# Optimization experiments

Measured on AMD Instinct MI355X. Metric: run time of the kernel, lower is better.

Reference implementation:

```python
import jax, jax.numpy as jnp
import numpy as np

HIDDEN = 2048
ENGRAM = 256
ENTRIES = 32768
K = 3  # conv kernel size
LN_EPS = 1e-6
NORM_EPS = 1e-8
INV_TEMP = ENGRAM ** 0.5  # retrieval_temperature = 1/sqrt(engram_dim)
CLAMP_MIN = 0.5  # step 0 < clamp_until_step=800 -> hard clamp active


def _l2norm(x):
    n = jnp.linalg.norm(x, axis=-1, keepdims=True)
    return x / jnp.maximum(n, NORM_EPS)


def _rmsnorm(x, w, eps=LN_EPS):
    ms = jnp.mean(jnp.square(x), axis=-1, keepdims=True)
    return x * jax.lax.rsqrt(ms + eps) * w


def _layernorm(x, g, b, eps=LN_EPS):
    mu = jnp.mean(x, axis=-1, keepdims=True)
    var = jnp.mean(jnp.square(x - mu), axis=-1, keepdims=True)
    return (x - mu) * jax.lax.rsqrt(var + eps) * g + b


def setup_inputs() -> dict:
    key = jax.random.key(0)
    ks = jax.random.split(key, 7)
    s = lambda fan: 1.0 / np.sqrt(fan)
    return {
        "hidden_state": jax.random.normal(ks[0], (4, 1024, HIDDEN), jnp.float32),
        "table": jax.random.normal(ks[1], (ENTRIES, ENGRAM), jnp.float32),
        "Wq": jax.random.normal(ks[2], (HIDDEN, ENGRAM), jnp.float32) * s(HIDDEN),
        "ln_gamma": jnp.ones((ENGRAM,), jnp.float32),
        "ln_beta": jnp.zeros((ENGRAM,), jnp.float32),
        "Wk": jax.random.normal(ks[3], (ENGRAM, HIDDEN), jnp.float32) * s(ENGRAM),
        "Wv": jax.random.normal(ks[4], (ENGRAM, HIDDEN), jnp.float32) * s(ENGRAM),
        "gate_norm_w": jnp.ones((HIDDEN,), jnp.float32),
        "key_norm_w": jnp.ones((HIDDEN,), jnp.float32),
        # depthwise causal conv weight [C, K] (torch init zeros; randn for a meaningful test)
        "conv_w": jax.random.normal(ks[5], (HIDDEN, K), jnp.float32) * 0.1,
    }


def reference(hidden_state, table, Wq, ln_gamma, ln_beta, Wk, Wv,
              gate_norm_w, key_norm_w, conv_w):
    B, L, C = hidden_state.shape
    # --- retrieval: cosine-sim softmax attention over frozen table ---
    q = jnp.einsum('blc,ce->ble', hidden_state, Wq)
    qn = _l2norm(q)
    tn = _l2norm(table)
    sims = jnp.einsum('ble,te->blt', qn, tn)            # [B,L,T]
    weights = jax.nn.softmax(sims * INV_TEMP, axis=-1)
    retrieved = jnp.einsum('blt,te->ble', weights, table)
    retrieved = _layernorm(retrieved, ln_gamma, ln_beta)
    # --- key/value projections + gating ---
    key_ = jnp.einsum('ble,ec->blc', retrieved, Wk)
    value = jnp.einsum('ble,ec->blc', retrieved, Wv)
    h_norm = _rmsnorm(hidden_state, gate_norm_w)
    k_norm = _rmsnorm(key_, key_norm_w)
    dot = jnp.sum(h_norm * k_norm, axis=-1, keepdims=True)
    raw_gate = jax.nn.sigmoid(dot / np.sqrt(C).astype(np.float32))
    gate = jnp.maximum(raw_gate, CLAMP_MIN)             # clamp phase (step < 800)
    gated = gate * value                                 # [B,L,C]
    # --- causal depthwise conv along seq (left pad K-1) ---
    padded = jnp.pad(gated, ((0, 0), (K - 1, 0), (0, 0)))
    conv = sum(conv_w[:, k] * padded[:, k:k + L, :] for k in range(K))
    return jax.nn.silu(conv), gate
```

## Files before the change

kernel.cpp:

```cpp
#include <hip/hip_runtime.h>
#include <stdint.h>


#define NTOK 4096
#define CDIM 2048
#define EDIM 256
#define TROWS 32768
#define SPLIT 16
#define OUT0 (NTOK * CDIM)

typedef __attribute__((ext_vector_type(8))) short bf16x8;
typedef __attribute__((ext_vector_type(4))) float f32x4;

__device__ inline float bf2f(unsigned short u) { return __uint_as_float((unsigned)u << 16); }
__device__ inline unsigned short f2bf(float f) {
  unsigned x = __float_as_uint(f);
  x += 0x7fffu + ((x >> 16) & 1u);
  return (unsigned short)(x >> 16);
}
__device__ inline unsigned cvt_pk_bf16(float lo, float hi) {
  unsigned r;
  asm("v_cvt_pk_bf16_f32 %0, %1, %2" : "=v"(r) : "v"(lo), "v"(hi));
  return r;
}
__device__ inline void gll16(const void* g, void* l) {
  __builtin_amdgcn_global_load_lds((const __attribute__((address_space(1))) void*)g,
                                   (__attribute__((address_space(3))) void*)l, 16, 0, 0);
}

__global__ __launch_bounds__(256) void cast_bf16_kernel(
    const float* __restrict__ in, unsigned short* __restrict__ out) {
  const int idx = blockIdx.x * 256 + threadIdx.x;
  float4 v0 = *reinterpret_cast<const float4*>(&in[(size_t)idx * 8]);
  float4 v1 = *reinterpret_cast<const float4*>(&in[(size_t)idx * 8 + 4]);
  bf16x8 o;
  o[0] = (short)f2bf(v0.x); o[1] = (short)f2bf(v0.y);
  o[2] = (short)f2bf(v0.z); o[3] = (short)f2bf(v0.w);
  o[4] = (short)f2bf(v1.x); o[5] = (short)f2bf(v1.y);
  o[6] = (short)f2bf(v1.z); o[7] = (short)f2bf(v1.w);
  *reinterpret_cast<bf16x8*>(&out[(size_t)idx * 8]) = o;
}

__global__ __launch_bounds__(256) void transpose_cast_kernel(
    const float* __restrict__ in0, const float* __restrict__ in1,
    unsigned short* __restrict__ out, int R, int C) {
  __shared__ float lt[32][33];
  const int tid = threadIdx.x;
  const int r0 = blockIdx.x * 32, c0 = blockIdx.y * 32;
  const float* in = blockIdx.z ? in1 : in0;
  unsigned short* op = out + (size_t)blockIdx.z * R * C;
  {
    int r = tid >> 3, c4 = (tid & 7) * 4;
    float4 v = *reinterpret_cast<const float4*>(&in[(size_t)(r0 + r) * C + c0 + c4]);
    lt[r][c4] = v.x; lt[r][c4 + 1] = v.y; lt[r][c4 + 2] = v.z; lt[r][c4 + 3] = v.w;
  }
  __syncthreads();
  {
    int c = tid >> 3, r4 = (tid & 7) * 4;
#pragma unroll
    for (int j = 0; j < 4; ++j)
      op[(size_t)(c0 + c) * R + r0 + r4 + j] = f2bf(lt[r4 + j][c]);
  }
}

__global__ __launch_bounds__(256) void tabprep_kernel(
    const float* __restrict__ table, unsigned short* __restrict__ tnb,
    unsigned short* __restrict__ tvb) {
  __shared__ float lt[32][257];
  __shared__ float inv[32];
  const int tid = threadIdx.x, nb = blockIdx.x;
  const int r0 = nb * 32;
#pragma unroll
  for (int i = 0; i < 8; ++i) {
    int id = i * 256 + tid;
    int row = id >> 6, e4 = (id & 63) * 4;
    float4 v = *reinterpret_cast<const float4*>(&table[(size_t)(r0 + row) * EDIM + e4]);
    lt[row][e4] = v.x; lt[row][e4 + 1] = v.y; lt[row][e4 + 2] = v.z; lt[row][e4 + 3] = v.w;
  }
  __syncthreads();
  {
    int row = tid >> 3, sub = tid & 7;
    float ss = 0.f;
#pragma unroll
    for (int j = 0; j < 32; ++j) { float v = lt[row][sub + 8 * j]; ss = fmaf(v, v, ss); }
    ss += __shfl_xor(ss, 1); ss += __shfl_xor(ss, 2); ss += __shfl_xor(ss, 4);
    if (sub == 0) inv[row] = 1.f / fmaxf(sqrtf(ss), 1e-8f);
  }
  __syncthreads();
#pragma unroll
  for (int i = 0; i < 4; ++i) {
    int q = i * 256 + tid;
    {
      int c8 = q >> 5, row = q & 31;
      bf16x8 v;
#pragma unroll
      for (int j = 0; j < 8; ++j) v[j] = (short)f2bf(lt[row][c8 * 8 + j] * inv[row]);
      *reinterpret_cast<bf16x8*>(&tnb[(size_t)nb * 8192 + q * 8]) = v;
    }
    {
      int hi = q >> 8, e = q & 255;
      bf16x8 v;
#pragma unroll
      for (int j = 0; j < 8; ++j) v[j] = (short)f2bf(lt[hi * 8 + j][e]);
      *reinterpret_cast<bf16x8*>(&tvb[(size_t)nb * 8192 + q * 8]) = v;
    }
  }
}

template <bool F32OUT>
__global__ __launch_bounds__(256, 2) void gemm_bt_kernel(
    const unsigned short* __restrict__ A, const unsigned short* __restrict__ BT,
    void* __restrict__ Cout, int M, int N, int Kfull, int klen) {
  __shared__ alignas(16) unsigned short sA[2][128 * 64];
  __shared__ alignas(16) unsigned short sB[2][128 * 64];
  const int tid = threadIdx.x;
  const int lane = tid & 63;
  const int wave = tid >> 6;
  const int laneLo = lane & 15, laneHi = lane >> 4;
  const int nbn = N >> 7;
  const int bm = blockIdx.x / nbn, bn = blockIdx.x % nbn;
  const int koff = blockIdx.y * klen;
  const int wr = wave >> 1, wc = wave & 1;
  f32x4 acc[4][4];
#pragma unroll
  for (int m = 0; m < 4; ++m)
#pragma unroll
    for (int n = 0; n < 4; ++n) acc[m][n] = (f32x4){0.f, 0.f, 0.f, 0.f};
  const int nkt = klen >> 6;
  auto STAGE = [&](int b, int kt) {
#pragma unroll
    for (int i = 0; i < 4; ++i) {
      int q = i * 256 + tid;
      int row = q >> 3, cl = q & 7;
      int cs = cl ^ (row & 7);
      gll16(A + ((size_t)(bm * 128 + row) * Kfull + koff + kt * 64 + cs * 8), &sA[b][q * 8]);
      gll16(BT + ((size_t)(bn * 128 + row) * Kfull + koff + kt * 64 + cs * 8), &sB[b][q * 8]);
    }
  };
  STAGE(0, 0);
  for (int kt = 0; kt < nkt; ++kt) {
    __syncthreads();
    if (kt + 1 < nkt) STAGE((kt & 1) ^ 1, kt + 1);
    const unsigned short* pA = sA[kt & 1];
    const unsigned short* pB = sB[kt & 1];
#pragma unroll
    for (int ks = 0; ks < 2; ++ks) {
      bf16x8 af[4], bfr[4];
#pragma unroll
      for (int m = 0; m < 4; ++m) {
        int row = wr * 64 + m * 16 + laneLo;
        af[m] = *reinterpret_cast<const bf16x8*>(&pA[(row * 8 + ((ks * 4 + laneHi) ^ (row & 7))) * 8]);
      }
#pragma unroll
      for (int n = 0; n < 4; ++n) {
        int row = wc * 64 + n * 16 + laneLo;
        bfr[n] = *reinterpret_cast<const bf16x8*>(&pB[(row * 8 + ((ks * 4 + laneHi) ^ (row & 7))) * 8]);
      }
#pragma unroll
      for (int m = 0; m < 4; ++m)
#pragma unroll
        for (int n = 0; n < 4; ++n)
          acc[m][n] = __builtin_amdgcn_mfma_f32_16x16x32_bf16(af[m], bfr[n], acc[m][n], 0, 0, 0);
    }
  }
#pragma unroll
  for (int m = 0; m < 4; ++m)
#pragma unroll
    for (int n = 0; n < 4; ++n)
#pragma unroll
      for (int r = 0; r < 4; ++r) {
        size_t idx = (size_t)(bm * 128 + wr * 64 + m * 16 + laneHi * 4 + r) * N +
                     bn * 128 + wc * 64 + n * 16 + laneLo;
        if (F32OUT)
          ((float*)Cout)[(size_t)blockIdx.y * M * N + idx] = acc[m][n][r];
        else
          ((unsigned short*)Cout)[idx] = f2bf(acc[m][n][r]);
      }
}

__global__ __launch_bounds__(256) void qcombine_kernel(
    const float* __restrict__ qpart, unsigned short* __restrict__ qn) {
  __shared__ float red[4];
  const int t = blockIdx.x, e = threadIdx.x;
  const int wave = e >> 6, lane = e & 63;
  float v = qpart[(size_t)t * EDIM + e] + qpart[((size_t)NTOK + t) * EDIM + e];
  float ss = v * v;
#pragma unroll
  for (int m = 1; m <= 32; m <<= 1) ss += __shfl_xor(ss, m);
  if (lane == 0) red[wave] = ss;
  __syncthreads();
  ss = red[0] + red[1] + red[2] + red[3];
  const float inv = 1.f / fmaxf(sqrtf(ss), 1e-8f);
  qn[(size_t)t * EDIM + e] = f2bf(v * inv);
}

__global__ __launch_bounds__(256, 2) void attn_kernel(
    const unsigned short* __restrict__ qn, const unsigned short* __restrict__ tnb,
    const unsigned short* __restrict__ tvb, unsigned short* __restrict__ Opart,
    float* __restrict__ lpart) {
  __shared__ alignas(16) unsigned short bufK[2][8192];
  __shared__ alignas(16) unsigned short bufV[2][8192];
  __shared__ alignas(16) unsigned short pbuf[8][16][40];
  const int tid = threadIdx.x;
  const int wave = tid >> 6, lane = tid & 63;
  const int Lo = lane & 15, Hi = lane >> 4;
  const int cid = (blockIdx.x & 7) * 64 + (blockIdx.x >> 3);
  const int split = cid >> 5, tb = cid & 31;
  const int qkBase = tb * 128 + wave * 32;
  bf16x8 qf[2][8];
#pragma unroll
  for (int g = 0; g < 2; ++g)
#pragma unroll
    for (int ks = 0; ks < 8; ++ks)
      qf[g][ks] = *reinterpret_cast<const bf16x8*>(
          qn + (size_t)(qkBase + g * 16 + Lo) * EDIM + ks * 32 + Hi * 8);
  const int pvG = (wave & 1) * 4;
  const int pvF = (wave >> 1) * 8;
  f32x4 o[4][8];
#pragma unroll
  for (int ng = 0; ng < 4; ++ng)
#pragma unroll
    for (int f = 0; f < 8; ++f) o[ng][f] = (f32x4){0.f, 0.f, 0.f, 0.f};
  float l_run[2] = {0.f, 0.f};
  const int nt = (TROWS / SPLIT) / 32;
  const int nb0 = split * nt;
  auto STAGE = [&](int b, int blk) {
#pragma unroll
    for (int i = 0; i < 4; ++i) {
      int u = i * 256 + tid;
      gll16(tnb + (size_t)blk * 8192 + u * 8, &bufK[b][u * 8]);
      gll16(tvb + (size_t)blk * 8192 + u * 8, &bufV[b][u * 8]);
    }
  };
  STAGE(0, nb0);
  for (int it = 0; it < nt; ++it) {
    const int cur = it & 1;
    __syncthreads();
    f32x4 z00 = {0.f, 0.f, 0.f, 0.f}, z01 = z00, z10 = z00, z11 = z00;
    __builtin_amdgcn_s_setprio(1);
#pragma unroll
    for (int ks = 0; ks < 8; ++ks) {
      bf16x8 a0 = *reinterpret_cast<const bf16x8*>(&bufK[cur][((ks * 4 + Hi) * 32 + Lo) * 8]);
      bf16x8 a1 = *reinterpret_cast<const bf16x8*>(&bufK[cur][((ks * 4 + Hi) * 32 + 16 + Lo) * 8]);
      z00 = __builtin_amdgcn_mfma_f32_16x16x32_bf16(a0, qf[0][ks], z00, 0, 0, 0);
      z01 = __builtin_amdgcn_mfma_f32_16x16x32_bf16(a1, qf[0][ks], z01, 0, 0, 0);
      z10 = __builtin_amdgcn_mfma_f32_16x16x32_bf16(a0, qf[1][ks], z10, 0, 0, 0);
      z11 = __builtin_amdgcn_mfma_f32_16x16x32_bf16(a1, qf[1][ks], z11, 0, 0, 0);
    }
    __builtin_amdgcn_s_setprio(0);
#pragma unroll
    for (int g = 0; g < 2; ++g) {
      const f32x4 za = g ? z10 : z00;
      const f32x4 zb = g ? z11 : z01;
      float p[8];
#pragma unroll
      for (int r = 0; r < 4; ++r) {
        p[r] = __expf(fmaf(16.f, za[r], -16.f));
        p[4 + r] = __expf(fmaf(16.f, zb[r], -16.f));
      }
      l_run[g] += ((p[0] + p[1]) + (p[2] + p[3])) + ((p[4] + p[5]) + (p[6] + p[7]));
      unsigned short* pb = &pbuf[wave * 2 + g][Lo][0];
      *reinterpret_cast<uint2*>(pb + Hi * 4) =
          make_uint2(cvt_pk_bf16(p[0], p[1]), cvt_pk_bf16(p[2], p[3]));
      *reinterpret_cast<uint2*>(pb + 16 + Hi * 4) =
          make_uint2(cvt_pk_bf16(p[4], p[5]), cvt_pk_bf16(p[6], p[7]));
    }
    __syncthreads();
    if (it + 1 < nt) STAGE(cur ^ 1, nb0 + it + 1);
    bf16x8 pa0 = *reinterpret_cast<const bf16x8*>(&pbuf[pvG + 0][Lo][Hi * 8]);
    bf16x8 pa1 = *reinterpret_cast<const bf16x8*>(&pbuf[pvG + 1][Lo][Hi * 8]);
    bf16x8 pa2 = *reinterpret_cast<const bf16x8*>(&pbuf[pvG + 2][Lo][Hi * 8]);
    bf16x8 pa3 = *reinterpret_cast<const bf16x8*>(&pbuf[pvG + 3][Lo][Hi * 8]);
    __builtin_amdgcn_s_setprio(1);
#pragma unroll
    for (int f = 0; f < 8; ++f) {
      bf16x8 vb = *reinterpret_cast<const bf16x8*>(
          &bufV[cur][(Hi * 256 + (pvF + f) * 16 + Lo) * 8]);
      o[0][f] = __builtin_amdgcn_mfma_f32_16x16x32_bf16(pa0, vb, o[0][f], 0, 0, 0);
      o[1][f] = __builtin_amdgcn_mfma_f32_16x16x32_bf16(pa1, vb, o[1][f], 0, 0, 0);
      o[2][f] = __builtin_amdgcn_mfma_f32_16x16x32_bf16(pa2, vb, o[2][f], 0, 0, 0);
      o[3][f] = __builtin_amdgcn_mfma_f32_16x16x32_bf16(pa3, vb, o[3][f], 0, 0, 0);
    }
    __builtin_amdgcn_s_setprio(0);
  }
#pragma unroll
  for (int g = 0; g < 2; ++g) {
    float l = l_run[g];
    l += __shfl_xor(l, 16);
    l += __shfl_xor(l, 32);
    if (lane < 16) lpart[(size_t)split * NTOK + qkBase + g * 16 + Lo] = l;
  }
#pragma unroll
  for (int ng = 0; ng < 4; ++ng)
#pragma unroll
    for (int f = 0; f < 8; ++f)
#pragma unroll
      for (int r = 0; r < 4; ++r) {
        int token = tb * 128 + (pvG + ng) * 16 + Hi * 4 + r;
        Opart[((size_t)split * NTOK + token) * EDIM + (pvF + f) * 16 + Lo] =
            f2bf(o[ng][f][r]);
      }
}

__global__ __launch_bounds__(256) void combine_ln_kernel(
    const unsigned short* __restrict__ Opart, const float* __restrict__ lpart,
    const float* __restrict__ gamma, const float* __restrict__ beta,
    unsigned short* __restrict__ retr) {
  __shared__ float red[4][2];
  const int t = blockIdx.x, e = threadIdx.x;
  const int wave = e >> 6, lane = e & 63;
  float acc = 0.f, l = 0.f;
#pragma unroll
  for (int s = 0; s < SPLIT; ++s) {
    acc += bf2f(Opart[((size_t)s * NTOK + t) * EDIM + e]);
    l += lpart[(size_t)s * NTOK + t];
  }
  const float r = acc / l;
  float s1 = r, s2 = r * r;
#pragma unroll
  for (int m = 1; m <= 32; m <<= 1) { s1 += __shfl_xor(s1, m); s2 += __shfl_xor(s2, m); }
  if (lane == 0) { red[wave][0] = s1; red[wave][1] = s2; }
  __syncthreads();
  s1 = red[0][0] + red[1][0] + red[2][0] + red[3][0];
  s2 = red[0][1] + red[1][1] + red[2][1] + red[3][1];
  const float mu = s1 * (1.f / 256.f);
  const float var = s2 * (1.f / 256.f) - mu * mu;
  const float rs = rsqrtf(var + 1e-6f);
  retr[(size_t)t * EDIM + e] = f2bf((r - mu) * rs * gamma[e] + beta[e]);
}

__global__ __launch_bounds__(256) void gate_kernel(
    const float* __restrict__ hidden, const unsigned short* __restrict__ kv,
    const float* __restrict__ gw, const float* __restrict__ kwn,
    float* __restrict__ gate_out) {
  __shared__ float red[4][3];
  const int t = blockIdx.x, tid = threadIdx.x;
  const int wave = tid >> 6, lane = tid & 63;
  float ssh = 0.f, ssk = 0.f, shk = 0.f;
#pragma unroll
  for (int i = 0; i < 8; ++i) {
    int cc = tid + i * 256;
    float h = hidden[(size_t)t * CDIM + cc];
    float k = bf2f(kv[(size_t)t * 4096 + cc]);
    ssh = fmaf(h, h, ssh);
    ssk = fmaf(k, k, ssk);
    shk = fmaf(h * gw[cc], k * kwn[cc], shk);
  }
#pragma unroll
  for (int m = 1; m <= 32; m <<= 1) {
    ssh += __shfl_xor(ssh, m); ssk += __shfl_xor(ssk, m); shk += __shfl_xor(shk, m);
  }
  if (lane == 0) { red[wave][0] = ssh; red[wave][1] = ssk; red[wave][2] = shk; }
  __syncthreads();
  ssh = red[0][0] + red[1][0] + red[2][0] + red[3][0];
  ssk = red[0][1] + red[1][1] + red[2][1] + red[3][1];
  shk = red[0][2] + red[1][2] + red[2][2] + red[3][2];
  const float rsh = rsqrtf(ssh * (1.f / 2048.f) + 1e-6f);
  const float rsk = rsqrtf(ssk * (1.f / 2048.f) + 1e-6f);
  const float dot = rsh * rsk * shk;
  const float rg = 1.f / (1.f + __expf(-dot * 0.02209708691207961f));
  if (tid == 0) gate_out[t] = fmaxf(rg, 0.5f);
}

__global__ __launch_bounds__(256) void conv_kernel(
    const unsigned short* __restrict__ kv, const float* __restrict__ gate,
    const float* __restrict__ convw, float* __restrict__ out0) {
  const int bid = blockIdx.x, tid = threadIdx.x;
  const int t = (bid & 7) * 512 + (bid >> 3);
  const int l = t & 1023;
  const int c0 = tid * 8;
  const float gt2 = gate[t];
  const float gt1 = (l >= 1) ? gate[t - 1] : 0.f;
  const float gt0 = (l >= 2) ? gate[t - 2] : 0.f;
  bf16x8 vz;
#pragma unroll
  for (int j = 0; j < 8; ++j) vz[j] = 0;
  const unsigned short* vbase = kv + 2048;
  bf16x8 v2 = *reinterpret_cast<const bf16x8*>(vbase + (size_t)t * 4096 + c0);
  bf16x8 v1 = (l >= 1) ? *reinterpret_cast<const bf16x8*>(vbase + (size_t)(t - 1) * 4096 + c0) : vz;
  bf16x8 v0 = (l >= 2) ? *reinterpret_cast<const bf16x8*>(vbase + (size_t)(t - 2) * 4096 + c0) : vz;
  float res[8];
#pragma unroll
  for (int j = 0; j < 8; ++j) {
    int c = c0 + j;
    float x = convw[c * 3 + 0] * (gt0 * bf2f((unsigned short)v0[j]))
            + convw[c * 3 + 1] * (gt1 * bf2f((unsigned short)v1[j]))
            + convw[c * 3 + 2] * (gt2 * bf2f((unsigned short)v2[j]));
    res[j] = x / (1.f + __expf(-x));
  }
  *reinterpret_cast<float4*>(out0 + (size_t)t * CDIM + c0) =
      make_float4(res[0], res[1], res[2], res[3]);
  *reinterpret_cast<float4*>(out0 + (size_t)t * CDIM + c0 + 4) =
      make_float4(res[4], res[5], res[6], res[7]);
}

extern "C" void kernel_launch(void* const* d_in, const int* in_sizes, int n_in,
                              void* d_out, int out_size, void* d_ws, size_t ws_size,
                              hipStream_t stream) {
  const float* hidden = (const float*)d_in[0];
  const float* table  = (const float*)d_in[1];
  const float* Wq     = (const float*)d_in[2];
  const float* ln_g   = (const float*)d_in[3];
  const float* ln_b   = (const float*)d_in[4];
  const float* Wk     = (const float*)d_in[5];
  const float* Wv     = (const float*)d_in[6];
  const float* gnw    = (const float*)d_in[7];
  const float* knw    = (const float*)d_in[8];
  const float* convw  = (const float*)d_in[9];
  float* out = (float*)d_out;

  char* w = (char*)d_ws;
  const size_t MB = 1u << 20;
  unsigned short* tnb    = (unsigned short*)(w);
  unsigned short* tvb    = (unsigned short*)(w + 16 * MB);
  unsigned short* kv     = (unsigned short*)(w);
  unsigned short* qn     = (unsigned short*)(w + 32 * MB);
  unsigned short* retr   = (unsigned short*)(w + 32 * MB);
  unsigned short* WkvT   = (unsigned short*)(w + 34 * MB);
  float*          lpart  = (float*)(w + 36 * MB);
  unsigned short* Opart  = (unsigned short*)(w + 37 * MB);
  unsigned short* hb     = (unsigned short*)(w + 37 * MB);
  unsigned short* WqT    = (unsigned short*)(w + 53 * MB);
  float*          qpart  = (float*)(w + 54 * MB);

  cast_bf16_kernel<<<NTOK * CDIM / 2048, 256, 0, stream>>>(hidden, hb);
  transpose_cast_kernel<<<dim3(64, 8, 1), 256, 0, stream>>>(Wq, Wq, WqT, CDIM, EDIM);
  transpose_cast_kernel<<<dim3(8, 64, 2), 256, 0, stream>>>(Wk, Wv, WkvT, EDIM, CDIM);
  tabprep_kernel<<<TROWS / 32, 256, 0, stream>>>(table, tnb, tvb);
  gemm_bt_kernel<true><<<dim3((NTOK / 128) * (EDIM / 128), 2), 256, 0, stream>>>(
      hb, WqT, qpart, NTOK, EDIM, CDIM, 1024);
  qcombine_kernel<<<NTOK, 256, 0, stream>>>(qpart, qn);
  attn_kernel<<<32 * SPLIT, 256, 0, stream>>>(qn, tnb, tvb, Opart, lpart);
  combine_ln_kernel<<<NTOK, 256, 0, stream>>>(Opart, lpart, ln_g, ln_b, retr);
  gemm_bt_kernel<false><<<dim3((NTOK / 128) * (2 * CDIM / 128), 1), 256, 0, stream>>>(
      retr, WkvT, kv, NTOK, 2 * CDIM, EDIM, EDIM);
  gate_kernel<<<NTOK, 256, 0, stream>>>(hidden, kv, gnw, knw, out + OUT0);
  conv_kernel<<<NTOK, 256, 0, stream>>>(kv, out + OUT0, convw, out);
}
```

Before: 220.3 us.

## Fuse hidden-state bf16 cast into Q GEMM and software-pipeline attention PV

Removes the standalone cast kernel and instead loads fp32 hidden states in the Q-projection GEMM, converting to bf16 in registers before writing into LDS. This drops one full write and read of the bf16 copy, at the cost of synchronous loads replacing async global-to-LDS loads. The attention loop is also restructured: V loads are staged separately from K, and the previous tile's P·V MFMAs run after the current tile's QK and exp. This cuts one barrier per iteration and overlaps the PV compute with the softmax stage.

```diff
diff --git a/kernel.cpp b/kernel.cpp
--- a/kernel.cpp
+++ b/kernel.cpp
@@ -26,19 +26,6 @@
 __device__ inline void gll16(const void* g, void* l) {
   __builtin_amdgcn_global_load_lds((const __attribute__((address_space(1))) void*)g,
                                    (__attribute__((address_space(3))) void*)l, 16, 0, 0);
-}
-
-__global__ __launch_bounds__(256) void cast_bf16_kernel(
-    const float* __restrict__ in, unsigned short* __restrict__ out) {
-  const int idx = blockIdx.x * 256 + threadIdx.x;
-  float4 v0 = *reinterpret_cast<const float4*>(&in[(size_t)idx * 8]);
-  float4 v1 = *reinterpret_cast<const float4*>(&in[(size_t)idx * 8 + 4]);
-  bf16x8 o;
-  o[0] = (short)f2bf(v0.x); o[1] = (short)f2bf(v0.y);
-  o[2] = (short)f2bf(v0.z); o[3] = (short)f2bf(v0.w);
-  o[4] = (short)f2bf(v1.x); o[5] = (short)f2bf(v1.y);
-  o[6] = (short)f2bf(v1.z); o[7] = (short)f2bf(v1.w);
-  *reinterpret_cast<bf16x8*>(&out[(size_t)idx * 8]) = o;
 }
 
 __global__ __launch_bounds__(256) void transpose_cast_kernel(
@@ -107,9 +94,9 @@
   }
 }
 
-template <bool F32OUT>
+template <bool F32OUT, bool AF32>
 __global__ __launch_bounds__(256, 2) void gemm_bt_kernel(
-    const unsigned short* __restrict__ A, const unsigned short* __restrict__ BT,
+    const void* __restrict__ Ain, const unsigned short* __restrict__ BT,
     void* __restrict__ Cout, int M, int N, int Kfull, int klen) {
   __shared__ alignas(16) unsigned short sA[2][128 * 64];
   __shared__ alignas(16) unsigned short sB[2][128 * 64];
@@ -133,7 +120,22 @@
       int q = i * 256 + tid;
       int row = q >> 3, cl = q & 7;
       int cs = cl ^ (row & 7);
-      gll16(A + ((size_t)(bm * 128 + row) * Kfull + koff + kt * 64 + cs * 8), &sA[b][q * 8]);
+      if constexpr (AF32) {
+        const float* src = (const float*)Ain +
+            ((size_t)(bm * 128 + row) * Kfull + koff + kt * 64 + cs * 8);
+        float4 x = *reinterpret_cast<const float4*>(src);
+        float4 y = *reinterpret_cast<const float4*>(src + 4);
+        bf16x8 v;
+        v[0] = (short)f2bf(x.x); v[1] = (short)f2bf(x.y);
+        v[2] = (short)f2bf(x.z); v[3] = (short)f2bf(x.w);
+        v[4] = (short)f2bf(y.x); v[5] = (short)f2bf(y.y);
+        v[6] = (short)f2bf(y.z); v[7] = (short)f2bf(y.w);
+        *reinterpret_cast<bf16x8*>(&sA[b][q * 8]) = v;
+      } else {
+        gll16((const unsigned short*)Ain +
+                  ((size_t)(bm * 128 + row) * Kfull + koff + kt * 64 + cs * 8),
+              &sA[b][q * 8]);
+      }
       gll16(BT + ((size_t)(bn * 128 + row) * Kfull + koff + kt * 64 + cs * 8), &sB[b][q * 8]);
     }
   };
@@ -224,18 +226,41 @@
   float l_run[2] = {0.f, 0.f};
   const int nt = (TROWS / SPLIT) / 32;
   const int nb0 = split * nt;
-  auto STAGE = [&](int b, int blk) {
+  auto STAGE_K = [&](int b, int blk) {
 #pragma unroll
     for (int i = 0; i < 4; ++i) {
       int u = i * 256 + tid;
       gll16(tnb + (size_t)blk * 8192 + u * 8, &bufK[b][u * 8]);
+    }
+  };
+  auto STAGE_V = [&](int b, int blk) {
+#pragma unroll
+    for (int i = 0; i < 4; ++i) {
+      int u = i * 256 + tid;
       gll16(tvb + (size_t)blk * 8192 + u * 8, &bufV[b][u * 8]);
     }
   };
-  STAGE(0, nb0);
+  auto PV = [&](const unsigned short* vb0) {
+    bf16x8 pa0 = *reinterpret_cast<const bf16x8*>(&pbuf[pvG + 0][Lo][Hi * 8]);
+    bf16x8 pa1 = *reinterpret_cast<const bf16x8*>(&pbuf[pvG + 1][Lo][Hi * 8]);
+    bf16x8 pa2 = *reinterpret_cast<const bf16x8*>(&pbuf[pvG + 2][Lo][Hi * 8]);
+    bf16x8 pa3 = *reinterpret_cast<const bf16x8*>(&pbuf[pvG + 3][Lo][Hi * 8]);
+#pragma unroll
+    for (int f = 0; f < 8; ++f) {
+      bf16x8 vb = *reinterpret_cast<const bf16x8*>(
+          &vb0[(Hi * 256 + (pvF + f) * 16 + Lo) * 8]);
+      o[0][f] = __builtin_amdgcn_mfma_f32_16x16x32_bf16(pa0, vb, o[0][f], 0, 0, 0);
+      o[1][f] = __builtin_amdgcn_mfma_f32_16x16x32_bf16(pa1, vb, o[1][f], 0, 0, 0);
+      o[2][f] = __builtin_amdgcn_mfma_f32_16x16x32_bf16(pa2, vb, o[2][f], 0, 0, 0);
+      o[3][f] = __builtin_amdgcn_mfma_f32_16x16x32_bf16(pa3, vb, o[3][f], 0, 0, 0);
+    }
+  };
+  STAGE_K(0, nb0);
   for (int it = 0; it < nt; ++it) {
     const int cur = it & 1;
     __syncthreads();
+    if (it + 1 < nt) STAGE_K(cur ^ 1, nb0 + it + 1);
+    STAGE_V(cur ^ 1, nb0 + it);
     f32x4 z00 = {0.f, 0.f, 0.f, 0.f}, z01 = z00, z10 = z00, z11 = z00;
     __builtin_amdgcn_s_setprio(1);
 #pragma unroll
@@ -248,6 +273,7 @@
       z11 = __builtin_amdgcn_mfma_f32_16x16x32_bf16(a1, qf[1][ks], z11, 0, 0, 0);
     }
     __builtin_amdgcn_s_setprio(0);
+    uint2 pw[2][2];
 #pragma unroll
     for (int g = 0; g < 2; ++g) {
       const f32x4 za = g ? z10 : z00;
@@ -259,30 +285,26 @@
         p[4 + r] = __expf(fmaf(16.f, zb[r], -16.f));
       }
       l_run[g] += ((p[0] + p[1]) + (p[2] + p[3])) + ((p[4] + p[5]) + (p[6] + p[7]));
+      pw[g][0] = make_uint2(cvt_pk_bf16(p[0], p[1]), cvt_pk_bf16(p[2], p[3]));
+      pw[g][1] = make_uint2(cvt_pk_bf16(p[4], p[5]), cvt_pk_bf16(p[6], p[7]));
+    }
+    if (it > 0) {
+      __builtin_amdgcn_s_setprio(1);
+      PV(bufV[cur]);
+      __builtin_amdgcn_s_setprio(0);
+    }
+    asm volatile("s_waitcnt lgkmcnt(0)\n\ts_barrier" ::: "memory");
+#pragma unroll
+    for (int g = 0; g < 2; ++g) {
       unsigned short* pb = &pbuf[wave * 2 + g][Lo][0];
-      *reinterpret_cast<uint2*>(pb + Hi * 4) =
-          make_uint2(cvt_pk_bf16(p[0], p[1]), cvt_pk_bf16(p[2], p[3]));
-      *reinterpret_cast<uint2*>(pb + 16 + Hi * 4) =
-          make_uint2(cvt_pk_bf16(p[4], p[5]), cvt_pk_bf16(p[6], p[7]));
-    }
-    __syncthreads();
-    if (it + 1 < nt) STAGE(cur ^ 1, nb0 + it + 1);
-    bf16x8 pa0 = *reinterpret_cast<const bf16x8*>(&pbuf[pvG + 0][Lo][Hi * 8]);
-    bf16x8 pa1 = *reinterpret_cast<const bf16x8*>(&pbuf[pvG + 1][Lo][Hi * 8]);
-    bf16x8 pa2 = *reinterpret_cast<const bf16x8*>(&pbuf[pvG + 2][Lo][Hi * 8]);
-    bf16x8 pa3 = *reinterpret_cast<const bf16x8*>(&pbuf[pvG + 3][Lo][Hi * 8]);
-    __builtin_amdgcn_s_setprio(1);
-#pragma unroll
-    for (int f = 0; f < 8; ++f) {
-      bf16x8 vb = *reinterpret_cast<const bf16x8*>(
-          &bufV[cur][(Hi * 256 + (pvF + f) * 16 + Lo) * 8]);
-      o[0][f] = __builtin_amdgcn_mfma_f32_16x16x32_bf16(pa0, vb, o[0][f], 0, 0, 0);
-      o[1][f] = __builtin_amdgcn_mfma_f32_16x16x32_bf16(pa1, vb, o[1][f], 0, 0, 0);
-      o[2][f] = __builtin_amdgcn_mfma_f32_16x16x32_bf16(pa2, vb, o[2][f], 0, 0, 0);
-      o[3][f] = __builtin_amdgcn_mfma_f32_16x16x32_bf16(pa3, vb, o[3][f], 0, 0, 0);
-    }
-    __builtin_amdgcn_s_setprio(0);
-  }
+      *reinterpret_cast<uint2*>(pb + Hi * 4) = pw[g][0];
+      *reinterpret_cast<uint2*>(pb + 16 + Hi * 4) = pw[g][1];
+    }
+  }
+  __syncthreads();
+  __builtin_amdgcn_s_setprio(1);
+  PV(bufV[nt & 1]);
+  __builtin_amdgcn_s_setprio(0);
 #pragma unroll
   for (int g = 0; g < 2; ++g) {
     float l = l_run[g];
@@ -419,20 +441,18 @@
   unsigned short* WkvT   = (unsigned short*)(w + 34 * MB);
   float*          lpart  = (float*)(w + 36 * MB);
   unsigned short* Opart  = (unsigned short*)(w + 37 * MB);
-  unsigned short* hb     = (unsigned short*)(w + 37 * MB);
   unsigned short* WqT    = (unsigned short*)(w + 53 * MB);
   float*          qpart  = (float*)(w + 54 * MB);
 
-  cast_bf16_kernel<<<NTOK * CDIM / 2048, 256, 0, stream>>>(hidden, hb);
   transpose_cast_kernel<<<dim3(64, 8, 1), 256, 0, stream>>>(Wq, Wq, WqT, CDIM, EDIM);
   transpose_cast_kernel<<<dim3(8, 64, 2), 256, 0, stream>>>(Wk, Wv, WkvT, EDIM, CDIM);
   tabprep_kernel<<<TROWS / 32, 256, 0, stream>>>(table, tnb, tvb);
-  gemm_bt_kernel<true><<<dim3((NTOK / 128) * (EDIM / 128), 2), 256, 0, stream>>>(
-      hb, WqT, qpart, NTOK, EDIM, CDIM, 1024);
+  gemm_bt_kernel<true, true><<<dim3((NTOK / 128) * (EDIM / 128), 2), 256, 0, stream>>>(
+      hidden, WqT, qpart, NTOK, EDIM, CDIM, 1024);
   qcombine_kernel<<<NTOK, 256, 0, stream>>>(qpart, qn);
   attn_kernel<<<32 * SPLIT, 256, 0, stream>>>(qn, tnb, tvb, Opart, lpart);
   combine_ln_kernel<<<NTOK, 256, 0, stream>>>(Opart, lpart, ln_g, ln_b, retr);
-  gemm_bt_kernel<false><<<dim3((NTOK / 128) * (2 * CDIM / 128), 1), 256, 0, stream>>>(
+  gemm_bt_kernel<false, false><<<dim3((NTOK / 128) * (2 * CDIM / 128), 1), 256, 0, stream>>>(
       retr, WkvT, kv, NTOK, 2 * CDIM, EDIM, EDIM);
   gate_kernel<<<NTOK, 256, 0, stream>>>(hidden, kv, gnw, knw, out + OUT0);
   conv_kernel<<<NTOK, 256, 0, stream>>>(kv, out + OUT0, convw, out);
```

After: 226.6 us. 2.8% more time.
